# Performance work log

Measured on AMD Instinct MI355X. Metric: run time of the kernel, lower is better.

Reference implementation:

```python
import jax, jax.numpy as jnp
import numpy as np

B, T, V, E, H, L = 32, 128, 32000, 512, 512, 3
EPS = 1e-5


def setup_inputs() -> dict:
    key = jax.random.key(0)
    ks = jax.random.split(key, 6)
    idx = jax.random.randint(ks[0], (B, T), 0, V, dtype=jnp.int32)
    emb = jax.random.normal(ks[1], (V, E), dtype=jnp.float32) * 0.02
    # packed gate weights per layer: columns ordered [forget, input, candidate, output]
    # acting on concat([h_prev, x]) of width H+E (matches torch cat order)
    W = jax.random.normal(ks[2], (L, H + E, 4 * H), dtype=jnp.float32) * (1.0 / np.sqrt(H + E))
    b = jnp.zeros((L, 4 * H), dtype=jnp.float32)
    gamma = jnp.ones((H,), dtype=jnp.float32)
    beta = jnp.zeros((H,), dtype=jnp.float32)
    Wh = jax.random.normal(ks[3], (H, V), dtype=jnp.float32) * 0.02
    bh = jnp.zeros((V,), dtype=jnp.float32)
    return {"idx": idx, "emb": emb, "W": W, "b": b, "gamma": gamma, "beta": beta, "Wh": Wh, "bh": bh}


def _lstm_out(idx, emb, W, b):
    x = emb[idx]                       # [B, T, E]
    h0 = jnp.zeros((L, B, H), dtype=x.dtype)
    c0 = jnp.zeros((L, B, H), dtype=x.dtype)

    def step(carry, x_t):
        h, c = carry                   # each [L, B, H]
        new_h, new_c = [], []
        inp = x_t                      # [B, E]
        for i in range(L):
            concat = jnp.concatenate([h[i], inp], axis=1)      # [B, H+E]
            gates = concat @ W[i] + b[i]                       # [B, 4H]
            f, ig, g, o = jnp.split(gates, 4, axis=1)
            f = jax.nn.sigmoid(f)
            ig = jax.nn.sigmoid(ig)
            g = jnp.tanh(g)
            o = jax.nn.sigmoid(o)
            ci = f * c[i] + ig * g
            hi = o * jnp.tanh(ci)
            new_h.append(hi)
            new_c.append(ci)
            inp = hi
        return (jnp.stack(new_h), jnp.stack(new_c)), inp

    _, outs = jax.lax.scan(step, (h0, c0), jnp.swapaxes(x, 0, 1))  # outs: [T, B, H]
    return jnp.swapaxes(outs, 0, 1)    # [B, T, H]


def reference(idx, emb, W, b, gamma, beta, Wh, bh):
    out = _lstm_out(idx, emb, W, b)
    mu = out.mean(-1, keepdims=True)
    var = out.var(-1, keepdims=True)
    out = (out - mu) / jnp.sqrt(var + EPS) * gamma + beta       # LayerNorm
    logits = out @ Wh + bh                                      # [B, T, V]
    return logits
```

## Files before the change

kernel.cpp:

```cpp
#include <hip/hip_runtime.h>

typedef unsigned short u16;
typedef unsigned int u32;
typedef __attribute__((ext_vector_type(8))) __bf16 bf16x8;
typedef __attribute__((ext_vector_type(4))) float f32x4;

#define B_ 32
#define T_ 128
#define V_ 32000
#define H_ 512
#define L_ 3
#define LW 64

__device__ __forceinline__ u16 f2bf(float x) {
  union { float f; u32 u; } v; v.f = x;
  u32 r = v.u + 0x7fffu + ((v.u >> 16) & 1u);
  return (u16)(r >> 16);
}
__device__ __forceinline__ float b2f(u16 h) {
  union { u32 u; float f; } v; v.u = ((u32)h) << 16; return v.f;
}
__device__ __forceinline__ float sigf(float x) { return 1.f / (1.f + __expf(-x)); }
__device__ __forceinline__ float tanhf_(float x) { return 2.f / (1.f + __expf(-2.f * x)) - 1.f; }

__device__ __forceinline__ void gload16(const void* g, void* l) {
  __builtin_amdgcn_global_load_lds((const __attribute__((address_space(1))) u32*)g,
                                   (__attribute__((address_space(3))) u32*)l, 16, 0, 0);
}

union F4B8 { f32x4 f; bf16x8 b; uint4 u; };

__device__ __forceinline__ void load16_sc1(const void* p, F4B8* dst) {
  asm volatile("global_load_dwordx4 %0, %1, off sc1" : "=v"(dst->f) : "v"(p));
}
__device__ __forceinline__ void store_short_sc1(void* p, u32 v) {
  asm volatile("global_store_short %0, %1, off sc1" :: "v"(p), "v"(v));
}

__device__ __forceinline__ bool frags_dirty(const F4B8* r, int n) {
  u32 acc = 0;
#pragma unroll
  for (int i = 0; i < 16; ++i) {
    if (i < n) acc |= r[i].u.x | r[i].u.y | r[i].u.z | r[i].u.w;
  }
  return __ballot((acc & 0x40004000u) != 0u) != 0ull;
}

__global__ __launch_bounds__(64) void k_embed(const int* __restrict__ idx,
                                              const float* __restrict__ emb,
                                              u16* __restrict__ X) {
  int bt = blockIdx.x;
  int b = bt >> 7, t = bt & 127;
  int v = idx[bt];
  const float* src = emb + (size_t)v * H_;
  u16* dst = X + ((size_t)t * B_ + b) * H_;
  int l8 = threadIdx.x << 3;
  float4 f0 = *(const float4*)(src + l8);
  float4 f1 = *(const float4*)(src + l8 + 4);
  uint4 o;
  o.x = (u32)f2bf(f0.x) | ((u32)f2bf(f0.y) << 16);
  o.y = (u32)f2bf(f0.z) | ((u32)f2bf(f0.w) << 16);
  o.z = (u32)f2bf(f1.x) | ((u32)f2bf(f1.y) << 16);
  o.w = (u32)f2bf(f1.z) | ((u32)f2bf(f1.w) << 16);
  *(uint4*)(dst + l8) = o;
}

__global__ __launch_bounds__(256) void k_transpose(const float* __restrict__ Wh,
                                                   u16* __restrict__ WhT) {
  __shared__ u16 tile[64][66];
  int nb = blockIdx.x % 500, kb = blockIdx.x / 500;
  int n0 = nb << 6, k0 = kb << 6;
  int tid = threadIdx.x;
#pragma unroll
  for (int it = 0; it < 16; ++it) {
    int k = (it << 2) + (tid >> 6);
    int n = tid & 63;
    tile[k][n] = f2bf(Wh[(size_t)(k0 + k) * V_ + n0 + n]);
  }
  __syncthreads();
#pragma unroll
  for (int it = 0; it < 16; ++it) {
    int n = (it << 2) + (tid >> 6);
    int k = tid & 63;
    WhT[(size_t)(n0 + n) * H_ + k0 + k] = tile[k][n];
  }
}

__global__ __launch_bounds__(128, 1) void k_lstm(const float* __restrict__ Wg,
                                                 const float* __restrict__ bias,
                                                 const u16* __restrict__ X,
                                                 u16* __restrict__ Hbuf) {
  __shared__ u16 bfrag[32][2][64][8];
  const int l = blockIdx.x / LW, g = blockIdx.x % LW;
  const int tid = threadIdx.x, wave = tid >> 6, lane = tid & 63;

  const float* Wl = Wg + (size_t)l * 1024 * 2048;
  for (int f = tid; f < 4096; f += 128) {
    int kb = f >> 7, nt = (f >> 6) & 1, ln = f & 63;
    int n = (nt << 4) + (ln & 15);
    int col = ((n >> 3) << 9) + (g << 3) + (n & 7);
    int k0 = (kb << 5) + ((ln >> 4) << 3);
#pragma unroll
    for (int j = 0; j < 8; ++j)
      bfrag[kb][nt][ln][j] = f2bf(Wl[(size_t)(k0 + j) * 2048 + col]);
  }
  __syncthreads();
  bf16x8 wfh[16][2], wfx[16][2];
#pragma unroll
  for (int kb = 0; kb < 16; ++kb) {
    wfh[kb][0] = *(const bf16x8*)&bfrag[kb][0][lane][0];
    wfh[kb][1] = *(const bf16x8*)&bfrag[kb][1][lane][0];
    wfx[kb][0] = *(const bf16x8*)&bfrag[16 + kb][0][lane][0];
    wfx[kb][1] = *(const bf16x8*)&bfrag[16 + kb][1][lane][0];
  }

  const int jj = lane & 7, cg = (g << 3) + jj;
  const float bF = bias[l * 2048 + cg];
  const float bI = bias[l * 2048 + 512 + cg];
  const float bG = bias[l * 2048 + 1024 + cg];
  const float bO = bias[l * 2048 + 1536 + cg];
  float cst[4] = {0.f, 0.f, 0.f, 0.f};

  const size_t slice = (size_t)B_ * H_;
  u16* Hl = Hbuf + (size_t)l * (T_ + 1) * slice;
  const u16* inb = (l == 0) ? X : (Hbuf + (size_t)(l - 1) * (T_ + 1) * slice + slice);

  const int mrow = (wave << 4) + (lane & 15);
  const int koff = ((lane >> 4) << 3);

  f32x4 z = {0.f, 0.f, 0.f, 0.f};
  f32x4 pxA0 = z, pxA1 = z, pxB0 = z, pxB1 = z;

  auto do_x = [&](int t) {
    const u16* xin = inb + (size_t)t * slice + (size_t)mrow * H_ + koff;
    F4B8 ax[16];
    if (l == 0) {
#pragma unroll
      for (int kb = 0; kb < 16; ++kb) ax[kb].b = *(const bf16x8*)(xin + (kb << 5));
    } else {
      for (;;) {
#pragma unroll
        for (int kb = 0; kb < 16; ++kb) load16_sc1(xin + (kb << 5), &ax[kb]);
        asm volatile("s_waitcnt vmcnt(0)" ::: "memory");
        __builtin_amdgcn_sched_barrier(0);
        if (!frags_dirty(ax, 16)) break;
      }
    }
    pxA0 = z; pxA1 = z; pxB0 = z; pxB1 = z;
#pragma unroll
    for (int kb = 0; kb < 16; kb += 2) {
      pxA0 = __builtin_amdgcn_mfma_f32_16x16x32_bf16(ax[kb].b, wfx[kb][0], pxA0, 0, 0, 0);
      pxA1 = __builtin_amdgcn_mfma_f32_16x16x32_bf16(ax[kb].b, wfx[kb][1], pxA1, 0, 0, 0);
      pxB0 = __builtin_amdgcn_mfma_f32_16x16x32_bf16(ax[kb + 1].b, wfx[kb + 1][0], pxB0, 0, 0, 0);
      pxB1 = __builtin_amdgcn_mfma_f32_16x16x32_bf16(ax[kb + 1].b, wfx[kb + 1][1], pxB1, 0, 0, 0);
    }
  };

  do_x(0);

  for (int t = 0; t < T_; ++t) {
    f32x4 hA0 = z, hA1 = z, hB0 = z, hB1 = z;
    f32x4 hC0 = z, hC1 = z, hD0 = z, hD1 = z;
    if (t > 0) {
      const u16* hin = Hl + (size_t)t * slice + (size_t)mrow * H_ + koff;
      F4B8 ah[16];
      for (;;) {
#pragma unroll
        for (int kb = 0; kb < 16; ++kb) load16_sc1(hin + (kb << 5), &ah[kb]);
        asm volatile("s_waitcnt vmcnt(0)" ::: "memory");
        __builtin_amdgcn_sched_barrier(0);
        if (!frags_dirty(ah, 16)) break;
      }
#pragma unroll
      for (int kb = 0; kb < 16; kb += 4) {
        hA0 = __builtin_amdgcn_mfma_f32_16x16x32_bf16(ah[kb].b, wfh[kb][0], hA0, 0, 0, 0);
        hA1 = __builtin_amdgcn_mfma_f32_16x16x32_bf16(ah[kb].b, wfh[kb][1], hA1, 0, 0, 0);
        hB0 = __builtin_amdgcn_mfma_f32_16x16x32_bf16(ah[kb + 1].b, wfh[kb + 1][0], hB0, 0, 0, 0);
        hB1 = __builtin_amdgcn_mfma_f32_16x16x32_bf16(ah[kb + 1].b, wfh[kb + 1][1], hB1, 0, 0, 0);
        hC0 = __builtin_amdgcn_mfma_f32_16x16x32_bf16(ah[kb + 2].b, wfh[kb + 2][0], hC0, 0, 0, 0);
        hC1 = __builtin_amdgcn_mfma_f32_16x16x32_bf16(ah[kb + 2].b, wfh[kb + 2][1], hC1, 0, 0, 0);
        hD0 = __builtin_amdgcn_mfma_f32_16x16x32_bf16(ah[kb + 3].b, wfh[kb + 3][0], hD0, 0, 0, 0);
        hD1 = __builtin_amdgcn_mfma_f32_16x16x32_bf16(ah[kb + 3].b, wfh[kb + 3][1], hD1, 0, 0, 0);
      }
    }
    {
      f32x4 s0, s1, q0, q1;
#pragma unroll
      for (int r = 0; r < 4; ++r) {
        s0[r] = pxA0[r] + pxB0[r] + ((hA0[r] + hB0[r]) + (hC0[r] + hD0[r]));
        s1[r] = pxA1[r] + pxB1[r] + ((hA1[r] + hB1[r]) + (hC1[r] + hD1[r]));
      }
#pragma unroll
      for (int r = 0; r < 4; ++r) { q0[r] = __shfl_xor(s0[r], 8); q1[r] = __shfl_xor(s1[r], 8); }
      const bool lo = (lane & 8) == 0;
      float hv[4];
#pragma unroll
      for (int r = 0; r < 4; ++r) {
        float fr = lo ? s0[r] : q0[r];
        float ir = lo ? q0[r] : s0[r];
        float gr = lo ? s1[r] : q1[r];
        float orr = lo ? q1[r] : s1[r];
        float cc = sigf(fr + bF) * cst[r] + sigf(ir + bI) * tanhf_(gr + bG);
        cst[r] = cc;
        hv[r] = sigf(orr + bO) * tanhf_(cc);
      }
      if (lo) {
        int rbase = (wave << 4) + ((lane >> 4) << 2);
        u16* hp = Hl + (size_t)(t + 1) * slice + cg;
#pragma unroll
        for (int r = 0; r < 4; ++r)
          store_short_sc1(hp + (size_t)(rbase + r) * H_, (u32)f2bf(hv[r]));
      }
    }
    if (t + 1 < T_) do_x(t + 1);
  }
}

__global__ __launch_bounds__(64) void k_ln(const u16* __restrict__ H2,
                                           const float* __restrict__ gamma,
                                           const float* __restrict__ beta,
                                           u16* __restrict__ Aln) {
  int bt = blockIdx.x;
  int b = bt >> 7, t = bt & 127;
  const u16* src = H2 + ((size_t)(t + 1) * B_ + b) * H_;
  int l8 = threadIdx.x << 3;
  uint4 r = *(const uint4*)(src + l8);
  float v[8];
  v[0] = b2f(r.x & 0xffff); v[1] = b2f(r.x >> 16);
  v[2] = b2f(r.y & 0xffff); v[3] = b2f(r.y >> 16);
  v[4] = b2f(r.z & 0xffff); v[5] = b2f(r.z >> 16);
  v[6] = b2f(r.w & 0xffff); v[7] = b2f(r.w >> 16);
  float s = 0.f, sq = 0.f;
#pragma unroll
  for (int i = 0; i < 8; ++i) { s += v[i]; sq += v[i] * v[i]; }
#pragma unroll
  for (int off = 32; off > 0; off >>= 1) {
    s += __shfl_xor(s, off);
    sq += __shfl_xor(sq, off);
  }
  float mu = s * (1.f / 512.f);
  float inv = rsqrtf(sq * (1.f / 512.f) - mu * mu + 1e-5f);
  float4 g0 = *(const float4*)(gamma + l8), g1 = *(const float4*)(gamma + l8 + 4);
  float4 be0 = *(const float4*)(beta + l8), be1 = *(const float4*)(beta + l8 + 4);
  float gg[8] = {g0.x, g0.y, g0.z, g0.w, g1.x, g1.y, g1.z, g1.w};
  float bb[8] = {be0.x, be0.y, be0.z, be0.w, be1.x, be1.y, be1.z, be1.w};
  u16 o16[8];
#pragma unroll
  for (int i = 0; i < 8; ++i) o16[i] = f2bf((v[i] - mu) * inv * gg[i] + bb[i]);
  uint4 o;
  o.x = (u32)o16[0] | ((u32)o16[1] << 16);
  o.y = (u32)o16[2] | ((u32)o16[3] << 16);
  o.z = (u32)o16[4] | ((u32)o16[5] << 16);
  o.w = (u32)o16[6] | ((u32)o16[7] << 16);
  *(uint4*)(Aln + (size_t)bt * H_ + l8) = o;
}

__global__ __launch_bounds__(256) void k_gemm(const u16* __restrict__ A,
                                              const u16* __restrict__ Bt,
                                              const float* __restrict__ bh,
                                              float* __restrict__ C) {
  __shared__ u16 As[128 * 64], Bs[128 * 64];
  const int bid = blockIdx.x;
  const int mb = bid / 250, nb = bid % 250;
  const size_t arow0 = (size_t)mb << 7;
  const size_t bcol0 = (size_t)nb << 7;
  const int tid = threadIdx.x, wave = tid >> 6, lane = tid & 63;
  const int wm = wave & 1, wn = wave >> 1;
  f32x4 acc[4][4];
  f32x4 z = {0.f, 0.f, 0.f, 0.f};
#pragma unroll
  for (int i = 0; i < 4; ++i)
#pragma unroll
    for (int jj = 0; jj < 4; ++jj) acc[i][jj] = z;

  for (int kt = 0; kt < 8; ++kt) {
#pragma unroll
    for (int it = 0; it < 4; ++it) {
      int rb = (it << 5) + (wave << 3);
      int r = rb + (lane >> 3);
      int kc = ((lane & 7) << 3);
      gload16(A + (arow0 + r) * H_ + (kt << 6) + kc, &As[rb << 6]);
      gload16(Bt + (bcol0 + r) * H_ + (kt << 6) + kc, &Bs[rb << 6]);
    }
    __syncthreads();
#pragma unroll
    for (int kb = 0; kb < 2; ++kb) {
      bf16x8 af[4], bf[4];
#pragma unroll
      for (int mi = 0; mi < 4; ++mi)
        af[mi] = *(const bf16x8*)&As[(((wm << 6) + (mi << 4) + (lane & 15)) << 6) + (kb << 5) + ((lane >> 4) << 3)];
#pragma unroll
      for (int ni = 0; ni < 4; ++ni)
        bf[ni] = *(const bf16x8*)&Bs[(((wn << 6) + (ni << 4) + (lane & 15)) << 6) + (kb << 5) + ((lane >> 4) << 3)];
#pragma unroll
      for (int mi = 0; mi < 4; ++mi)
#pragma unroll
        for (int ni = 0; ni < 4; ++ni)
          acc[mi][ni] = __builtin_amdgcn_mfma_f32_16x16x32_bf16(af[mi], bf[ni], acc[mi][ni], 0, 0, 0);
    }
    __syncthreads();
  }
  const int rb4 = ((lane >> 4) << 2), n0 = lane & 15;
#pragma unroll
  for (int ni = 0; ni < 4; ++ni) {
    size_t col = bcol0 + (wn << 6) + (ni << 4) + n0;
    float bv = bh[col];
#pragma unroll
    for (int mi = 0; mi < 4; ++mi) {
      size_t row = arow0 + (wm << 6) + (mi << 4) + rb4;
#pragma unroll
      for (int r = 0; r < 4; ++r)
        C[(row + r) * V_ + col] = acc[mi][ni][r] + bv;
    }
  }
}

extern "C" void kernel_launch(void* const* d_in, const int* in_sizes, int n_in,
                              void* d_out, int out_size, void* d_ws, size_t ws_size,
                              hipStream_t stream) {
  const int* idx = (const int*)d_in[0];
  const float* emb = (const float*)d_in[1];
  const float* Wg = (const float*)d_in[2];
  const float* bias = (const float*)d_in[3];
  const float* gamma = (const float*)d_in[4];
  const float* beta = (const float*)d_in[5];
  const float* Wh = (const float*)d_in[6];
  const float* bh = (const float*)d_in[7];
  float* out = (float*)d_out;

  char* ws = (char*)d_ws;
  const size_t szX = (size_t)T_ * B_ * H_ * 2;
  const size_t szH = (size_t)L_ * (T_ + 1) * B_ * H_ * 2;
  const size_t szA = (size_t)B_ * T_ * H_ * 2;
  const size_t szW = (size_t)V_ * H_ * 2;
  u16* X = (u16*)ws;
  u16* Hbuf = (u16*)(ws + szX);
  u16* Aln = (u16*)(ws + szX + szH);
  u16* WhT = (u16*)(ws + szX + szH + szA);
  if (ws_size < szX + szH + szA + szW) return;

  const size_t slice = (size_t)B_ * H_;
  hipMemsetAsync(Hbuf, 0xFF, szH, stream);
  for (int l = 0; l < L_; ++l)
    hipMemsetAsync(Hbuf + (size_t)l * (T_ + 1) * slice, 0, slice * 2, stream);
  k_embed<<<B_ * T_, 64, 0, stream>>>(idx, emb, X);
  k_transpose<<<500 * 8, 256, 0, stream>>>(Wh, WhT);
  k_lstm<<<L_ * LW, 128, 0, stream>>>(Wg, bias, X, Hbuf);
  k_ln<<<B_ * T_, 64, 0, stream>>>(Hbuf + (size_t)2 * (T_ + 1) * B_ * H_, gamma, beta, Aln);
  k_gemm<<<32 * 250, 256, 0, stream>>>(Aln, WhT, bh, out);
}
```

Baseline: 761.1 us.

## Rewrite vocab projection GEMM with 256x256 tiles, triple-buffered LDS and swizzle

The output projection GEMM moves from 128x128 tiles with 256 threads and a single LDS buffer to 256x256 tiles with 512 threads, a 3-stage LDS ring with K-step 32, and an XOR swizzle on the LDS layout. Global-to-LDS loads for step kt+2 are issued between the MFMA batches, and s_setprio raises wave priority around the MFMA work. The goal is to overlap memory with compute, raise data reuse per tile and cut LDS bank conflicts. The cost is more registers and LDS per block, which may lower occupancy. A small cleanup also simplifies frags_dirty.

Measured after the change: 732.1 us. 1.04x faster.

```diff
diff --git a/kernel.cpp b/kernel.cpp
--- a/kernel.cpp
+++ b/kernel.cpp
@@ -37,12 +37,10 @@
   asm volatile("global_store_short %0, %1, off sc1" :: "v"(p), "v"(v));
 }
 
-__device__ __forceinline__ bool frags_dirty(const F4B8* r, int n) {
+__device__ __forceinline__ bool frags_dirty(const F4B8* r) {
   u32 acc = 0;
 #pragma unroll
-  for (int i = 0; i < 16; ++i) {
-    if (i < n) acc |= r[i].u.x | r[i].u.y | r[i].u.z | r[i].u.w;
-  }
+  for (int i = 0; i < 16; ++i) acc |= r[i].u.x | r[i].u.y | r[i].u.z | r[i].u.w;
   return __ballot((acc & 0x40004000u) != 0u) != 0ull;
 }
 
@@ -143,7 +141,7 @@
         for (int kb = 0; kb < 16; ++kb) load16_sc1(xin + (kb << 5), &ax[kb]);
         asm volatile("s_waitcnt vmcnt(0)" ::: "memory");
         __builtin_amdgcn_sched_barrier(0);
-        if (!frags_dirty(ax, 16)) break;
+        if (!frags_dirty(ax)) break;
       }
     }
     pxA0 = z; pxA1 = z; pxB0 = z; pxB1 = z;
@@ -169,7 +167,7 @@
         for (int kb = 0; kb < 16; ++kb) load16_sc1(hin + (kb << 5), &ah[kb]);
         asm volatile("s_waitcnt vmcnt(0)" ::: "memory");
         __builtin_amdgcn_sched_barrier(0);
-        if (!frags_dirty(ah, 16)) break;
+        if (!frags_dirty(ah)) break;
       }
 #pragma unroll
       for (int kb = 0; kb < 16; kb += 4) {
@@ -255,59 +253,100 @@
   *(uint4*)(Aln + (size_t)bt * H_ + l8) = o;
 }
 
-__global__ __launch_bounds__(256) void k_gemm(const u16* __restrict__ A,
-                                              const u16* __restrict__ Bt,
-                                              const float* __restrict__ bh,
-                                              float* __restrict__ C) {
-  __shared__ u16 As[128 * 64], Bs[128 * 64];
-  const int bid = blockIdx.x;
-  const int mb = bid / 250, nb = bid % 250;
-  const size_t arow0 = (size_t)mb << 7;
-  const size_t bcol0 = (size_t)nb << 7;
+__global__ __launch_bounds__(512, 2) void k_gemm(const u16* __restrict__ A,
+                                                 const u16* __restrict__ Bt,
+                                                 const float* __restrict__ bh,
+                                                 float* __restrict__ C) {
+  __shared__ u16 As[3][256 * 32];
+  __shared__ u16 Bs[3][256 * 32];
   const int tid = threadIdx.x, wave = tid >> 6, lane = tid & 63;
-  const int wm = wave & 1, wn = wave >> 1;
-  f32x4 acc[4][4];
+  const int mb = blockIdx.x / 125, nb = blockIdx.x % 125;
+  const size_t arow0 = (size_t)mb << 8, bcol0 = (size_t)nb << 8;
+  const int wm = wave >> 2, wn = wave & 3;
+
+  const int srow = tid >> 2;
+  const int sq = (tid & 3) << 4;
+  const int sx = ((srow >> 1) & 3) << 4;
+  const int sqg = (sq ^ sx) >> 1;
+  const u16* Arow0 = A + (arow0 + srow) * H_ + sqg;
+  const u16* Arow1 = A + (arow0 + 128 + srow) * H_ + sqg;
+  const u16* Brow0 = Bt + (bcol0 + srow) * H_ + sqg;
+  const u16* Brow1 = Bt + (bcol0 + 128 + srow) * H_ + sqg;
+
+  const int rA = lane & 15, kg = lane >> 4;
+  const int ko = (((kg << 4) ^ (((rA >> 1) & 3) << 4)) >> 1);
+
+  f32x4 acc[8][4];
   f32x4 z = {0.f, 0.f, 0.f, 0.f};
 #pragma unroll
-  for (int i = 0; i < 4; ++i)
-#pragma unroll
-    for (int jj = 0; jj < 4; ++jj) acc[i][jj] = z;
-
-  for (int kt = 0; kt < 8; ++kt) {
-#pragma unroll
-    for (int it = 0; it < 4; ++it) {
-      int rb = (it << 5) + (wave << 3);
-      int r = rb + (lane >> 3);
-      int kc = ((lane & 7) << 3);
-      gload16(A + (arow0 + r) * H_ + (kt << 6) + kc, &As[rb << 6]);
-      gload16(Bt + (bcol0 + r) * H_ + (kt << 6) + kc, &Bs[rb << 6]);
-    }
-    __syncthreads();
-#pragma unroll
-    for (int kb = 0; kb < 2; ++kb) {
-      bf16x8 af[4], bf[4];
-#pragma unroll
-      for (int mi = 0; mi < 4; ++mi)
-        af[mi] = *(const bf16x8*)&As[(((wm << 6) + (mi << 4) + (lane & 15)) << 6) + (kb << 5) + ((lane >> 4) << 3)];
+  for (int i = 0; i < 8; ++i)
+#pragma unroll
+    for (int j = 0; j < 4; ++j) acc[i][j] = z;
+
+  auto stageA = [&](int kt, int c) {
+    gload16(Arow0 + (kt << 5), &As[c][wave << 9]);
+    gload16(Arow1 + (kt << 5), &As[c][4096 + (wave << 9)]);
+  };
+  auto stageB = [&](int kt, int c) {
+    gload16(Brow0 + (kt << 5), &Bs[c][wave << 9]);
+    gload16(Brow1 + (kt << 5), &Bs[c][4096 + (wave << 9)]);
+  };
+
+  stageA(0, 0); stageB(0, 0);
+  stageA(1, 1); stageB(1, 1);
+  asm volatile("s_waitcnt vmcnt(4)" ::: "memory");
+  __builtin_amdgcn_s_barrier();
+
+  for (int kt = 0; kt < 16; ++kt) {
+    const int c = kt % 3;
+    const bool pre = (kt + 2 <= 15);
+    const int c2 = (kt + 2) % 3;
+    bf16x8 bf[4], af[4];
+#pragma unroll
+    for (int ni = 0; ni < 4; ++ni)
+      bf[ni] = *(const bf16x8*)&Bs[c][((wn << 6) + (ni << 4) + rA) * 32 + ko];
+#pragma unroll
+    for (int mi = 0; mi < 4; ++mi)
+      af[mi] = *(const bf16x8*)&As[c][((wm << 7) + (mi << 4) + rA) * 32 + ko];
+    if (pre) stageA(kt + 2, c2);
+    __builtin_amdgcn_s_setprio(1);
+#pragma unroll
+    for (int mi = 0; mi < 4; ++mi)
 #pragma unroll
       for (int ni = 0; ni < 4; ++ni)
-        bf[ni] = *(const bf16x8*)&Bs[(((wn << 6) + (ni << 4) + (lane & 15)) << 6) + (kb << 5) + ((lane >> 4) << 3)];
-#pragma unroll
-      for (int mi = 0; mi < 4; ++mi)
-#pragma unroll
-        for (int ni = 0; ni < 4; ++ni)
-          acc[mi][ni] = __builtin_amdgcn_mfma_f32_16x16x32_bf16(af[mi], bf[ni], acc[mi][ni], 0, 0, 0);
-    }
-    __syncthreads();
-  }
-  const int rb4 = ((lane >> 4) << 2), n0 = lane & 15;
+        acc[mi][ni] = __builtin_amdgcn_mfma_f32_16x16x32_bf16(af[mi], bf[ni], acc[mi][ni], 0, 0, 0);
+    __builtin_amdgcn_s_setprio(0);
+    bf16x8 af2[4];
+#pragma unroll
+    for (int mi = 0; mi < 4; ++mi)
+      af2[mi] = *(const bf16x8*)&As[c][((wm << 7) + 64 + (mi << 4) + rA) * 32 + ko];
+    if (pre) stageB(kt + 2, c2);
+    __builtin_amdgcn_s_setprio(1);
+#pragma unroll
+    for (int mi = 0; mi < 4; ++mi)
+#pragma unroll
+      for (int ni = 0; ni < 4; ++ni)
+        acc[4 + mi][ni] = __builtin_amdgcn_mfma_f32_16x16x32_bf16(af2[mi], bf[ni], acc[4 + mi][ni], 0, 0, 0);
+    __builtin_amdgcn_s_setprio(0);
+    if (kt < 15) {
+      if (pre) {
+        asm volatile("s_waitcnt vmcnt(4)" ::: "memory");
+      } else {
+        asm volatile("s_waitcnt vmcnt(0)" ::: "memory");
+      }
+      __builtin_amdgcn_sched_barrier(0);
+      __builtin_amdgcn_s_barrier();
+    }
+  }
+
+  const int rb4 = (lane >> 4) << 2, n0 = lane & 15;
 #pragma unroll
   for (int ni = 0; ni < 4; ++ni) {
     size_t col = bcol0 + (wn << 6) + (ni << 4) + n0;
     float bv = bh[col];
 #pragma unroll
-    for (int mi = 0; mi < 4; ++mi) {
-      size_t row = arow0 + (wm << 6) + (mi << 4) + rb4;
+    for (int mi = 0; mi < 8; ++mi) {
+      size_t row = arow0 + (wm << 7) + (mi << 4) + rb4;
 #pragma unroll
       for (int r = 0; r < 4; ++r)
         C[(row + r) * V_ + col] = acc[mi][ni][r] + bv;
@@ -347,5 +386,5 @@
   k_transpose<<<500 * 8, 256, 0, stream>>>(Wh, WhT);
   k_lstm<<<L_ * LW, 128, 0, stream>>>(Wg, bias, X, Hbuf);
   k_ln<<<B_ * T_, 64, 0, stream>>>(Hbuf + (size_t)2 * (T_ + 1) * B_ * H_, gamma, beta, Aln);
-  k_gemm<<<32 * 250, 256, 0, stream>>>(Aln, WhT, bh, out);
-}
+  k_gemm<<<16 * 125, 512, 0, stream>>>(Aln, WhT, bh, out);
+}
```
